# Performance work log

Hardware: AMD Instinct MI355X
Metric: run time of the kernel (lower is better)

The kernel has to match this reference:

```python
import jax, jax.numpy as jnp
import numpy as np


def _lstm_dir(x, W_ih, W_hh, b_ih, b_hh, reverse):
    # x: [T, B, Din] -> hs: [T, B, H]; PyTorch gate order i,f,g,o
    xs = x[::-1] if reverse else x
    gx = xs @ W_ih.T + (b_ih + b_hh)  # [T, B, 4H] precomputed input contribution
    H = W_hh.shape[1]
    B = x.shape[1]

    def step(carry, g):
        h, c = carry
        g = g + h @ W_hh.T
        i, f, gg, o = jnp.split(g, 4, axis=-1)
        c = jax.nn.sigmoid(f) * c + jax.nn.sigmoid(i) * jnp.tanh(gg)
        h = jax.nn.sigmoid(o) * jnp.tanh(c)
        return (h, c), h

    z = jnp.zeros((B, H), x.dtype)
    _, hs = jax.lax.scan(step, (z, z), gx)
    return hs[::-1] if reverse else hs


def _emissions(inputs, emb, layers, W_out, b_out):
    x = jnp.swapaxes(emb[inputs], 0, 1)  # [T, B, E]
    for (Wif, Whf, bif, bhf, Wib, Whb, bib, bhb) in layers:
        hf = _lstm_dir(x, Wif, Whf, bif, bhf, False)
        hb = _lstm_dir(x, Wib, Whb, bib, bhb, True)
        x = jnp.concatenate([hf, hb], axis=-1)  # [T, B, 2H]
    return x @ W_out.T + b_out  # [T, B, K]


def _viterbi(em, start_trans, end_trans, trans):
    # em: [T, B, K] -> (tags [B, T] int32, best_score [B])
    score0 = start_trans + em[0]  # [B, K]

    def fwd_step(score, e):
        s = score[:, :, None] + trans[None, :, :]  # [B, Kprev, Knext]
        bp = jnp.argmax(s, axis=1)
        return jnp.max(s, axis=1) + e, bp

    score, bps = jax.lax.scan(fwd_step, score0, em[1:])  # bps: [T-1, B, K]
    score = score + end_trans
    last_tag = jnp.argmax(score, axis=1)  # [B]
    best_score = jnp.max(score, axis=1)   # [B]

    def back_step(tag, bp):
        prev = jnp.take_along_axis(bp, tag[:, None], axis=1)[:, 0]
        return prev, prev

    _, prevs = jax.lax.scan(back_step, last_tag, bps, reverse=True)  # [T-1, B]
    tags = jnp.concatenate([prevs, last_tag[None]], axis=0)  # [T, B]
    return jnp.swapaxes(tags, 0, 1).astype(jnp.int32), best_score


def setup_inputs() -> dict:
    key = jax.random.key(0)
    ks = jax.random.split(key, 24)
    B, T, V, E, H, K = 64, 512, 30000, 256, 256, 32

    def n(k, shape, s=0.05):
        return jax.random.normal(k, shape, dtype=jnp.float32) * s

    d = {"inputs": jax.random.randint(ks[0], (B, T), 0, V)}
    d["emb"] = n(ks[1], (V, E), 0.1).at[0].set(0.0)  # padding_idx=0
    i = 2
    for l, din in [(0, E), (1, 2 * H)]:
        for dr in ("f", "b"):
            d[f"W_ih_l{l}_{dr}"] = n(ks[i], (4 * H, din)); i += 1
            d[f"W_hh_l{l}_{dr}"] = n(ks[i], (4 * H, H)); i += 1
            d[f"b_ih_l{l}_{dr}"] = n(ks[i], (4 * H,)); i += 1
            d[f"b_hh_l{l}_{dr}"] = n(ks[i], (4 * H,)); i += 1
    d["W_out"] = n(ks[i], (K, 2 * H)); i += 1
    d["b_out"] = n(ks[i], (K,)); i += 1
    d["start_trans"] = n(ks[i], (K,)); i += 1
    d["end_trans"] = n(ks[i], (K,)); i += 1
    d["trans"] = n(ks[i], (K, K)); i += 1
    return d


def reference(inputs, emb,
              W_ih_l0_f, W_hh_l0_f, b_ih_l0_f, b_hh_l0_f,
              W_ih_l0_b, W_hh_l0_b, b_ih_l0_b, b_hh_l0_b,
              W_ih_l1_f, W_hh_l1_f, b_ih_l1_f, b_hh_l1_f,
              W_ih_l1_b, W_hh_l1_b, b_ih_l1_b, b_hh_l1_b,
              W_out, b_out, start_trans, end_trans, trans):
    layers = [
        (W_ih_l0_f, W_hh_l0_f, b_ih_l0_f, b_hh_l0_f,
         W_ih_l0_b, W_hh_l0_b, b_ih_l0_b, b_hh_l0_b),
        (W_ih_l1_f, W_hh_l1_f, b_ih_l1_f, b_hh_l1_f,
         W_ih_l1_b, W_hh_l1_b, b_ih_l1_b, b_hh_l1_b),
    ]
    em = _emissions(inputs, emb, layers, W_out, b_out)
    tags, _ = _viterbi(em, start_trans, end_trans, trans)
    return tags  # [B, T] best tag sequence per batch element
```

## Files before the change

### kernel.cpp

```cpp
#include <hip/hip_runtime.h>
#include <math.h>
#include <stdint.h>

#define TLEN 512
#define BSZ  64
#define EDIM 256
#define HDIM 256
#define GDIM 1024
#define KTAG 32

__device__ __forceinline__ float sigf(float x) { return 1.0f / (1.0f + expf(-x)); }

template<int KDIM, bool GATHER, bool TOXBUF>
__global__ __launch_bounds__(512, 2)
void lstm_fused(
    const float* __restrict__ gx_f, const float* __restrict__ gx_b,
    const float* __restrict__ Wf, const float* __restrict__ Wb,
    float* __restrict__ xout, float* __restrict__ hbuf,
    float* __restrict__ state, uint64_t* __restrict__ hxs,
    unsigned int fbase,
    int t0f, int t0b, int C, int init, int nlstm, int nmt,
    const float* __restrict__ A, const int* __restrict__ idx,
    const float* __restrict__ Bf, const float* __restrict__ Bb,
    const float* __restrict__ b1f, const float* __restrict__ b2f,
    const float* __restrict__ b1b, const float* __restrict__ b2b,
    float* __restrict__ ogx_f, float* __restrict__ ogx_b,
    int gt0f, int gt0b, int gr0f, int gr0b)
{
    __shared__ __align__(16) float h_lds[4][256];
    __shared__ __align__(16) float ps[2][4][256];
    __shared__ __align__(16) float gxs[4][256];
    __shared__ __align__(16) float As[8][132];
    __shared__ __align__(16) float Bs[8][132];

    const int bid = blockIdx.x;
    const int t = threadIdx.x;

    if (bid < nlstm) {
        const int cl  = bid & 31;
        const int rb  = bid >> 5;
        const int dir = cl >> 4;
        const int b0g = (cl & 15) * 4;
        const float* gx = dir ? gx_b : gx_f;
        const float* W  = dir ? Wb : Wf;
        const int t0 = dir ? t0b : t0f;

        const int rr = t & 255;
        const int kh = t >> 8;
        const int urow = ((rr >> 6) * 256) + rb * 64 + (rr & 63);

        float4 w[32];
        {
            const float4* wrow = (const float4*)(W + (size_t)urow * HDIM + kh * 128);
            #pragma unroll
            for (int i = 0; i < 32; ++i) w[i] = wrow[i];
        }
        #pragma unroll
        for (int i = 0; i < 32; ++i)
            asm volatile("" : "+v"(w[i].x), "+v"(w[i].y), "+v"(w[i].z), "+v"(w[i].w));

        float cc = 0.0f;
        for (int i = t; i < 4 * 256; i += 512) {
            int b = i >> 8, u = i & 255;
            h_lds[b][u] = init ? 0.0f
                : state[(((size_t)dir * BSZ + (b0g + b)) * 2) * HDIM + u];
        }
        if (t < 256) {
            int b = t >> 6, ug = rb * 64 + (t & 63);
            if (!init)
                cc = state[(((size_t)dir * BSZ + (b0g + b)) * 2) * HDIM + HDIM + ug];
        }
        __syncthreads();
        __builtin_amdgcn_s_setprio(1);

        for (int s = 0; s < C; ++s) {
            const int tloc = dir ? (C - 1 - s) : s;
            const int idx2 = t * 2;
            const int pb = idx2 >> 8;
            const int rem = idx2 & 255;
            const float* gxp = gx + ((size_t)tloc * BSZ + (b0g + pb)) * GDIM
                             + ((rem >> 6) * 256) + rb * 64 + (rem & 63);
            float2 gv = *(const float2*)gxp;
            float a0 = 0.f, a1 = 0.f, a2 = 0.f, a3 = 0.f;
            #pragma unroll
            for (int i = 0; i < 32; ++i) {
                float4 h0 = *(const float4*)&h_lds[0][kh * 128 + i * 4];
                float4 h1 = *(const float4*)&h_lds[1][kh * 128 + i * 4];
                float4 h2 = *(const float4*)&h_lds[2][kh * 128 + i * 4];
                float4 h3 = *(const float4*)&h_lds[3][kh * 128 + i * 4];
                a0 = fmaf(w[i].x, h0.x, a0); a0 = fmaf(w[i].y, h0.y, a0);
                a0 = fmaf(w[i].z, h0.z, a0); a0 = fmaf(w[i].w, h0.w, a0);
                a1 = fmaf(w[i].x, h1.x, a1); a1 = fmaf(w[i].y, h1.y, a1);
                a1 = fmaf(w[i].z, h1.z, a1); a1 = fmaf(w[i].w, h1.w, a1);
                a2 = fmaf(w[i].x, h2.x, a2); a2 = fmaf(w[i].y, h2.y, a2);
                a2 = fmaf(w[i].z, h2.z, a2); a2 = fmaf(w[i].w, h2.w, a2);
                a3 = fmaf(w[i].x, h3.x, a3); a3 = fmaf(w[i].y, h3.y, a3);
                a3 = fmaf(w[i].z, h3.z, a3); a3 = fmaf(w[i].w, h3.w, a3);
            }
            ps[kh][0][rr] = a0; ps[kh][1][rr] = a1;
            ps[kh][2][rr] = a2; ps[kh][3][rr] = a3;
            gxs[pb][rem] = gv.x; gxs[pb][rem + 1] = gv.y;
            __syncthreads();
            const unsigned want = fbase + (unsigned)(s + 1);
            if (t < 256) {
                const int b = t >> 6, u = t & 63;
                float pi = ps[0][b][u]       + ps[1][b][u]       + gxs[b][u];
                float pf = ps[0][b][64 + u]  + ps[1][b][64 + u]  + gxs[b][64 + u];
                float pg = ps[0][b][128 + u] + ps[1][b][128 + u] + gxs[b][128 + u];
                float po = ps[0][b][192 + u] + ps[1][b][192 + u] + gxs[b][192 + u];
                float iv = sigf(pi), fv = sigf(pf), gv2 = tanhf(pg), ov = sigf(po);
                cc = fv * cc + iv * gv2;
                float hv = ov * tanhf(cc);
                const int ug = rb * 64 + u;
                h_lds[b][ug] = hv;
                uint64_t pv = ((uint64_t)want << 32) | (uint64_t)__float_as_uint(hv);
                __hip_atomic_store(&hxs[(((size_t)(s & 1) * 32 + cl) * 4 + b) * 256 + ug],
                                   pv, __ATOMIC_RELAXED, __HIP_MEMORY_SCOPE_AGENT);
                if (TOXBUF)
                    xout[((size_t)(t0 + tloc) * BSZ + (b0g + b)) * 512 + dir * HDIM + ug] = hv;
                else
                    hbuf[(((size_t)dir * C + tloc) * BSZ + (b0g + b)) * HDIM + ug] = hv;
            }
            __builtin_amdgcn_s_setprio(0);
            #pragma unroll
            for (int q = 0; q < 2; ++q) {
                int i = t * 2 + q;
                int b = i >> 8, u = i & 255;
                if ((u >> 6) != rb) {
                    const uint64_t* src =
                        &hxs[(((size_t)(s & 1) * 32 + cl) * 4 + b) * 256 + u];
                    uint64_t v;
                    do {
                        v = __hip_atomic_load(src, __ATOMIC_RELAXED,
                                              __HIP_MEMORY_SCOPE_AGENT);
                    } while ((unsigned)(v >> 32) != want);
                    h_lds[b][u] = __uint_as_float((unsigned)v);
                }
            }
            __builtin_amdgcn_s_setprio(1);
            __syncthreads();
        }
        __builtin_amdgcn_s_setprio(0);
        if (t < 256) {
            int b = t >> 6, ug = rb * 64 + (t & 63);
            size_t sb = (((size_t)dir * BSZ + (b0g + b)) * 2) * HDIM;
            state[sb + ug] = h_lds[b][ug];
            state[sb + HDIM + ug] = cc;
        }
        return;
    }

    const int g = bid - nlstm;
    const int mx = g % nmt;
    const int ny = g / nmt;
    const int mt = mx * 128;
    const int ngc = ny * 128;
    const bool isF = (ngc < GDIM);
    const int nt = isF ? ngc : (ngc - GDIM);
    const float* Bw = isF ? Bf : Bb;
    const float* bias1 = isF ? b1f : b1b;
    const float* bias2 = isF ? b2f : b2b;
    float* Cc = isF ? ogx_f : ogx_b;
    const int t0 = isF ? gt0f : gt0b;
    const int r0 = isF ? gr0f : gr0b;

    const int tx = t & 15;
    const int ty = t >> 4;
    const int l_row = t >> 2;
    const int l_k = (t & 3) * 2;

    const float* arow;
    if (GATHER) {
        int m = mt + l_row;
        int tt = t0 + (m >> 6);
        int b = m & 63;
        arow = A + (size_t)idx[b * TLEN + tt] * (size_t)KDIM;
    } else {
        arow = A + (size_t)(r0 + mt + l_row) * (size_t)KDIM;
    }
    const float* brow = Bw + (size_t)(nt + l_row) * (size_t)KDIM;

    float acc[4][8];
    #pragma unroll
    for (int i = 0; i < 4; ++i)
        #pragma unroll
        for (int j = 0; j < 8; ++j) acc[i][j] = 0.0f;

    float2 av = *(const float2*)(arow + l_k);
    float2 bv = *(const float2*)(brow + l_k);
    for (int k0 = 0; k0 < KDIM; k0 += 8) {
        __syncthreads();
        As[l_k + 0][l_row] = av.x; As[l_k + 1][l_row] = av.y;
        Bs[l_k + 0][l_row] = bv.x; Bs[l_k + 1][l_row] = bv.y;
        __syncthreads();
        if (k0 + 8 < KDIM) {
            av = *(const float2*)(arow + k0 + 8 + l_k);
            bv = *(const float2*)(brow + k0 + 8 + l_k);
        }
        #pragma unroll
        for (int k = 0; k < 8; ++k) {
            float a[4], bb2[8];
            *(float4*)(a)       = *(const float4*)&As[k][ty * 4];
            *(float4*)(bb2)     = *(const float4*)&Bs[k][tx * 4];
            *(float4*)(bb2 + 4) = *(const float4*)&Bs[k][64 + tx * 4];
            #pragma unroll
            for (int i = 0; i < 4; ++i)
                #pragma unroll
                for (int j = 0; j < 8; ++j)
                    acc[i][j] = fmaf(a[i], bb2[j], acc[i][j]);
        }
    }

    float bs[8];
    #pragma unroll
    for (int j = 0; j < 4; ++j) bs[j] = bias1[nt + tx * 4 + j] + bias2[nt + tx * 4 + j];
    #pragma unroll
    for (int j = 4; j < 8; ++j) bs[j] = bias1[nt + 64 + tx * 4 + j - 4] + bias2[nt + 64 + tx * 4 + j - 4];
    #pragma unroll
    for (int i = 0; i < 4; ++i) {
        size_t row = (size_t)(mt + ty * 4 + i);
        float* cp0 = Cc + row * GDIM + nt + tx * 4;
        float* cp1 = Cc + row * GDIM + nt + 64 + tx * 4;
        *(float4*)cp0 = make_float4(acc[i][0] + bs[0], acc[i][1] + bs[1],
                                    acc[i][2] + bs[2], acc[i][3] + bs[3]);
        *(float4*)cp1 = make_float4(acc[i][4] + bs[4], acc[i][5] + bs[5],
                                    acc[i][6] + bs[6], acc[i][7] + bs[7]);
    }
}

__global__ __launch_bounds__(256)
void emis_part(const float* __restrict__ hbuf, const float* __restrict__ Wo,
               float* __restrict__ em_f, float* __restrict__ em_b,
               int t0f, int t0b, int C)
{
    __shared__ float Ws[128][33];
    const int dir = blockIdx.y;
    const int tid = threadIdx.x;
    const int r = tid >> 5;
    const int kk = tid & 31;
    const int mloc = blockIdx.x * 8 + r;
    const float* hrow = hbuf + ((size_t)dir * C * BSZ + mloc) * HDIM;
    float* emo = dir ? em_b : em_f;
    const int t0 = dir ? t0b : t0f;
    float acc = 0.0f;
    for (int kc = 0; kc < HDIM; kc += 128) {
        __syncthreads();
        for (int i = tid; i < KTAG * 128; i += 256) {
            int wk = i >> 7;
            int k = i & 127;
            Ws[k][wk] = Wo[(size_t)wk * 512 + dir * HDIM + kc + k];
        }
        __syncthreads();
        #pragma unroll 8
        for (int k4 = 0; k4 < 32; ++k4) {
            float4 xv = *(const float4*)(hrow + kc + k4 * 4);
            acc = fmaf(xv.x, Ws[k4 * 4 + 0][kk], acc);
            acc = fmaf(xv.y, Ws[k4 * 4 + 1][kk], acc);
            acc = fmaf(xv.z, Ws[k4 * 4 + 2][kk], acc);
            acc = fmaf(xv.w, Ws[k4 * 4 + 3][kk], acc);
        }
    }
    const int tloc = mloc >> 6;
    const int b = mloc & 63;
    emo[(((size_t)(t0 + tloc)) * BSZ + b) * KTAG + kk] = acc;
}

__global__ __launch_bounds__(64)
void viterbi(const float* __restrict__ em_f, const float* __restrict__ em_b,
             const float* __restrict__ bo,
             const float* __restrict__ st, const float* __restrict__ en,
             const float* __restrict__ tr, int* __restrict__ out)
{
    const int b = blockIdx.x;
    const int lane = threadIdx.x;
    __shared__ float s_tr[KTAG][KTAG + 1];
    __shared__ float s_sc[KTAG];
    __shared__ float s_fin[KTAG];
    __shared__ unsigned char s_bp[TLEN - 1][KTAG];
    for (int i = lane; i < KTAG * KTAG; i += 64)
        s_tr[i >> 5][i & 31] = tr[i];
    float eFn = 0.f, eBn = 0.f;
    if (lane < KTAG) {
        size_t e0 = (size_t)b * KTAG + lane;
        s_sc[lane] = st[lane] + em_f[e0] + em_b[e0] + bo[lane];
        size_t e1 = ((size_t)1 * BSZ + b) * KTAG + lane;
        eFn = em_f[e1]; eBn = em_b[e1];
    }
    __syncthreads();
    for (int t = 1; t < TLEN; ++t) {
        float ecF = eFn, ecB = eBn;
        if (t + 1 < TLEN && lane < KTAG) {
            size_t e2 = ((size_t)(t + 1) * BSZ + b) * KTAG + lane;
            eFn = em_f[e2]; eBn = em_b[e2];
        }
        float best = -3.0e38f;
        int arg = 0;
        if (lane < KTAG) {
            #pragma unroll
            for (int i = 0; i < KTAG; ++i) {
                float c = s_sc[i] + s_tr[i][lane];
                if (c > best) { best = c; arg = i; }
            }
        }
        __syncthreads();
        if (lane < KTAG) {
            s_sc[lane] = best + ecF + ecB + bo[lane];
            s_bp[t - 1][lane] = (unsigned char)arg;
        }
        __syncthreads();
    }
    if (lane < KTAG) s_fin[lane] = s_sc[lane] + en[lane];
    __syncthreads();
    if (lane == 0) {
        int tag = 0;
        float bv = s_fin[0];
        for (int i = 1; i < KTAG; ++i)
            if (s_fin[i] > bv) { bv = s_fin[i]; tag = i; }
        out[(size_t)b * TLEN + (TLEN - 1)] = tag;
        for (int t = TLEN - 2; t >= 0; --t) {
            tag = s_bp[t][tag];
            out[(size_t)b * TLEN + t] = tag;
        }
    }
}

extern "C" void kernel_launch(void* const* d_in, const int* in_sizes, int n_in,
                              void* d_out, int out_size, void* d_ws, size_t ws_size,
                              hipStream_t stream)
{
    (void)in_sizes; (void)n_in; (void)out_size;
    const int*   inputs     = (const int*)d_in[0];
    const float* emb        = (const float*)d_in[1];
    const float* W_ih_l0_f  = (const float*)d_in[2];
    const float* W_hh_l0_f  = (const float*)d_in[3];
    const float* b_ih_l0_f  = (const float*)d_in[4];
    const float* b_hh_l0_f  = (const float*)d_in[5];
    const float* W_ih_l0_b  = (const float*)d_in[6];
    const float* W_hh_l0_b  = (const float*)d_in[7];
    const float* b_ih_l0_b  = (const float*)d_in[8];
    const float* b_hh_l0_b  = (const float*)d_in[9];
    const float* W_ih_l1_f  = (const float*)d_in[10];
    const float* W_hh_l1_f  = (const float*)d_in[11];
    const float* b_ih_l1_f  = (const float*)d_in[12];
    const float* b_hh_l1_f  = (const float*)d_in[13];
    const float* W_ih_l1_b  = (const float*)d_in[14];
    const float* W_hh_l1_b  = (const float*)d_in[15];
    const float* b_ih_l1_b  = (const float*)d_in[16];
    const float* b_hh_l1_b  = (const float*)d_in[17];
    const float* W_out      = (const float*)d_in[18];
    const float* b_out      = (const float*)d_in[19];
    const float* start_tr   = (const float*)d_in[20];
    const float* end_tr     = (const float*)d_in[21];
    const float* trans      = (const float*)d_in[22];

    const size_t XBUF = 67108864ull;
    const size_t PERC = 4ull * 262144 + 131072;
    const size_t TAIL = 2ull * 4194304 + 524288 + 524288;
    int C = 8;
    for (int cand = TLEN; cand >= 8; cand >>= 1) {
        if (XBUF + (size_t)cand * PERC + TAIL <= ws_size) { C = cand; break; }
    }
    char* ws = (char*)d_ws;
    float* xbuf  = (float*)(ws);
    char*  p     = ws + XBUF;
    float* gxA_f = (float*)(p); p += (size_t)C * 262144;
    float* gxA_b = (float*)(p); p += (size_t)C * 262144;
    float* gxB_f = (float*)(p); p += (size_t)C * 262144;
    float* gxB_b = (float*)(p); p += (size_t)C * 262144;
    float* hbuf  = (float*)(p); p += (size_t)C * 131072;
    float* em_f  = (float*)(p); p += 4194304;
    float* em_b  = (float*)(p); p += 4194304;
    float* state = (float*)(p); p += 524288;
    uint64_t* hxs = (uint64_t*)(p);
    int* outi = (int*)d_out;

    const int nc = TLEN / C;
    const int nmt = C / 2;
    const int NG = nmt * 16;
    float* gxf[2] = { gxA_f, gxB_f };
    float* gxb[2] = { gxA_b, gxB_b };

    hipMemsetAsync(hxs, 0, 524288, stream);
    unsigned fbase = 0;

    lstm_fused<EDIM, true, true><<<NG, 512, 0, stream>>>(
        gxA_f, gxA_b, W_hh_l0_f, W_hh_l0_b, xbuf, nullptr, state, hxs, 0,
        0, 0, C, 1, 0, nmt,
        emb, inputs, W_ih_l0_f, W_ih_l0_b,
        b_ih_l0_f, b_hh_l0_f, b_ih_l0_b, b_hh_l0_b,
        gxA_f, gxA_b, 0, TLEN - C, 0, 0);
    for (int c = 0; c < nc; ++c) {
        int cur = c & 1, nxt = cur ^ 1;
        int hasN = (c + 1 < nc);
        int t0f = c * C, t0b = TLEN - (c + 1) * C;
        int g0f = (c + 1) * C, g0b = TLEN - (c + 2) * C;
        lstm_fused<EDIM, true, true><<<128 + (hasN ? NG : 0), 512, 0, stream>>>(
            gxf[cur], gxb[cur], W_hh_l0_f, W_hh_l0_b, xbuf, nullptr, state,
            hxs, fbase, t0f, t0b, C, c == 0 ? 1 : 0, 128, nmt,
            emb, inputs, W_ih_l0_f, W_ih_l0_b,
            b_ih_l0_f, b_hh_l0_f, b_ih_l0_b, b_hh_l0_b,
            gxf[nxt], gxb[nxt], g0f, g0b, 0, 0);
        fbase += (unsigned)C;
    }
    lstm_fused<512, false, false><<<NG, 512, 0, stream>>>(
        gxA_f, gxA_b, W_hh_l1_f, W_hh_l1_b, nullptr, hbuf, state, hxs, 0,
        0, 0, C, 1, 0, nmt,
        xbuf, nullptr, W_ih_l1_f, W_ih_l1_b,
        b_ih_l1_f, b_hh_l1_f, b_ih_l1_b, b_hh_l1_b,
        gxA_f, gxA_b, 0, TLEN - C, 0, (TLEN - C) * BSZ);
    for (int c = 0; c < nc; ++c) {
        int cur = c & 1, nxt = cur ^ 1;
        int hasN = (c + 1 < nc);
        int t0f = c * C, t0b = TLEN - (c + 1) * C;
        int g0f = (c + 1) * C, g0b = TLEN - (c + 2) * C;
        lstm_fused<512, false, false><<<128 + (hasN ? NG : 0), 512, 0, stream>>>(
            gxf[cur], gxb[cur], W_hh_l1_f, W_hh_l1_b, nullptr, hbuf, state,
            hxs, fbase, t0f, t0b, C, c == 0 ? 1 : 0, 128, nmt,
            xbuf, nullptr, W_ih_l1_f, W_ih_l1_b,
            b_ih_l1_f, b_hh_l1_f, b_ih_l1_b, b_hh_l1_b,
            gxf[nxt], gxb[nxt], g0f, g0b, g0f * BSZ, g0b * BSZ);
        fbase += (unsigned)C;
        dim3 ge(C * 8, 2);
        emis_part<<<ge, 256, 0, stream>>>(hbuf, W_out, em_f, em_b, t0f, t0b, C);
    }

    viterbi<<<64, 64, 0, stream>>>(em_f, em_b, b_out, start_tr, end_tr, trans,
                                   outi);
}
```

Before: 4.638 ms.

## Split recurrent LSTM work across 256 blocks with 4-way K split

Doubles the number of persistent recurrent blocks from 128 to 256. Each block now owns 32 hidden units instead of 64, and the K reduction is split four ways with 16 float4 weights per thread instead of 32. This halves per-block register weight storage and per-step FMA work, aiming to shorten the serial per-timestep critical path. In exchange, each block must poll more foreign hidden values from the global exchange buffer, and the reduction adds LDS partial sums.

```diff
diff --git a/kernel.cpp b/kernel.cpp
--- a/kernel.cpp
+++ b/kernel.cpp
@@ -28,8 +28,8 @@
     int gt0f, int gt0b, int gr0f, int gr0b)
 {
     __shared__ __align__(16) float h_lds[4][256];
-    __shared__ __align__(16) float ps[2][4][256];
-    __shared__ __align__(16) float gxs[4][256];
+    __shared__ __align__(16) float ps[4][4][128];
+    __shared__ __align__(16) float gxs[4][128];
     __shared__ __align__(16) float As[8][132];
     __shared__ __align__(16) float Bs[8][132];
 
@@ -45,18 +45,18 @@
         const float* W  = dir ? Wb : Wf;
         const int t0 = dir ? t0b : t0f;
 
-        const int rr = t & 255;
-        const int kh = t >> 8;
-        const int urow = ((rr >> 6) * 256) + rb * 64 + (rr & 63);
-
-        float4 w[32];
+        const int rr = t & 127;
+        const int kq = t >> 7;
+        const int urow = ((rr >> 5) * 256) + rb * 32 + (rr & 31);
+
+        float4 w[16];
         {
-            const float4* wrow = (const float4*)(W + (size_t)urow * HDIM + kh * 128);
+            const float4* wrow = (const float4*)(W + (size_t)urow * HDIM + kq * 64);
             #pragma unroll
-            for (int i = 0; i < 32; ++i) w[i] = wrow[i];
+            for (int i = 0; i < 16; ++i) w[i] = wrow[i];
         }
         #pragma unroll
-        for (int i = 0; i < 32; ++i)
+        for (int i = 0; i < 16; ++i)
             asm volatile("" : "+v"(w[i].x), "+v"(w[i].y), "+v"(w[i].z), "+v"(w[i].w));
 
         float cc = 0.0f;
@@ -65,8 +65,8 @@
             h_lds[b][u] = init ? 0.0f
                 : state[(((size_t)dir * BSZ + (b0g + b)) * 2) * HDIM + u];
         }
-        if (t < 256) {
-            int b = t >> 6, ug = rb * 64 + (t & 63);
+        if (t < 128) {
+            int b = t >> 5, ug = rb * 32 + (t & 31);
             if (!init)
                 cc = state[(((size_t)dir * BSZ + (b0g + b)) * 2) * HDIM + HDIM + ug];
         }
@@ -75,19 +75,15 @@
 
         for (int s = 0; s < C; ++s) {
             const int tloc = dir ? (C - 1 - s) : s;
-            const int idx2 = t * 2;
-            const int pb = idx2 >> 8;
-            const int rem = idx2 & 255;
-            const float* gxp = gx + ((size_t)tloc * BSZ + (b0g + pb)) * GDIM
-                             + ((rem >> 6) * 256) + rb * 64 + (rem & 63);
-            float2 gv = *(const float2*)gxp;
+            const int pb = t >> 7;
+            float gv = gx[((size_t)tloc * BSZ + (b0g + pb)) * GDIM + urow];
             float a0 = 0.f, a1 = 0.f, a2 = 0.f, a3 = 0.f;
             #pragma unroll
-            for (int i = 0; i < 32; ++i) {
-                float4 h0 = *(const float4*)&h_lds[0][kh * 128 + i * 4];
-                float4 h1 = *(const float4*)&h_lds[1][kh * 128 + i * 4];
-                float4 h2 = *(const float4*)&h_lds[2][kh * 128 + i * 4];
-                float4 h3 = *(const float4*)&h_lds[3][kh * 128 + i * 4];
+            for (int i = 0; i < 16; ++i) {
+                float4 h0 = *(const float4*)&h_lds[0][kq * 64 + i * 4];
+                float4 h1 = *(const float4*)&h_lds[1][kq * 64 + i * 4];
+                float4 h2 = *(const float4*)&h_lds[2][kq * 64 + i * 4];
+                float4 h3 = *(const float4*)&h_lds[3][kq * 64 + i * 4];
                 a0 = fmaf(w[i].x, h0.x, a0); a0 = fmaf(w[i].y, h0.y, a0);
                 a0 = fmaf(w[i].z, h0.z, a0); a0 = fmaf(w[i].w, h0.w, a0);
                 a1 = fmaf(w[i].x, h1.x, a1); a1 = fmaf(w[i].y, h1.y, a1);
@@ -97,21 +93,21 @@
                 a3 = fmaf(w[i].x, h3.x, a3); a3 = fmaf(w[i].y, h3.y, a3);
                 a3 = fmaf(w[i].z, h3.z, a3); a3 = fmaf(w[i].w, h3.w, a3);
             }
-            ps[kh][0][rr] = a0; ps[kh][1][rr] = a1;
-            ps[kh][2][rr] = a2; ps[kh][3][rr] = a3;
-            gxs[pb][rem] = gv.x; gxs[pb][rem + 1] = gv.y;
+            ps[kq][0][rr] = a0; ps[kq][1][rr] = a1;
+            ps[kq][2][rr] = a2; ps[kq][3][rr] = a3;
+            gxs[pb][rr] = gv;
             __syncthreads();
             const unsigned want = fbase + (unsigned)(s + 1);
-            if (t < 256) {
-                const int b = t >> 6, u = t & 63;
-                float pi = ps[0][b][u]       + ps[1][b][u]       + gxs[b][u];
-                float pf = ps[0][b][64 + u]  + ps[1][b][64 + u]  + gxs[b][64 + u];
-                float pg = ps[0][b][128 + u] + ps[1][b][128 + u] + gxs[b][128 + u];
-                float po = ps[0][b][192 + u] + ps[1][b][192 + u] + gxs[b][192 + u];
+            if (t < 128) {
+                const int b = t >> 5, ul = t & 31;
+                float pi = ps[0][b][ul]      + ps[1][b][ul]      + ps[2][b][ul]      + ps[3][b][ul]      + gxs[b][ul];
+                float pf = ps[0][b][32 + ul] + ps[1][b][32 + ul] + ps[2][b][32 + ul] + ps[3][b][32 + ul] + gxs[b][32 + ul];
+                float pg = ps[0][b][64 + ul] + ps[1][b][64 + ul] + ps[2][b][64 + ul] + ps[3][b][64 + ul] + gxs[b][64 + ul];
+                float po = ps[0][b][96 + ul] + ps[1][b][96 + ul] + ps[2][b][96 + ul] + ps[3][b][96 + ul] + gxs[b][96 + ul];
                 float iv = sigf(pi), fv = sigf(pf), gv2 = tanhf(pg), ov = sigf(po);
                 cc = fv * cc + iv * gv2;
                 float hv = ov * tanhf(cc);
-                const int ug = rb * 64 + u;
+                const int ug = rb * 32 + ul;
                 h_lds[b][ug] = hv;
                 uint64_t pv = ((uint64_t)want << 32) | (uint64_t)__float_as_uint(hv);
                 __hip_atomic_store(&hxs[(((size_t)(s & 1) * 32 + cl) * 4 + b) * 256 + ug],
@@ -124,9 +120,9 @@
             __builtin_amdgcn_s_setprio(0);
             #pragma unroll
             for (int q = 0; q < 2; ++q) {
-                int i = t * 2 + q;
+                int i = t + q * 512;
                 int b = i >> 8, u = i & 255;
-                if ((u >> 6) != rb) {
+                if ((u >> 5) != rb) {
                     const uint64_t* src =
                         &hxs[(((size_t)(s & 1) * 32 + cl) * 4 + b) * 256 + u];
                     uint64_t v;
@@ -141,8 +137,8 @@
             __syncthreads();
         }
         __builtin_amdgcn_s_setprio(0);
-        if (t < 256) {
-            int b = t >> 6, ug = rb * 64 + (t & 63);
+        if (t < 128) {
+            int b = t >> 5, ug = rb * 32 + (t & 31);
             size_t sb = (((size_t)dir * BSZ + (b0g + b)) * 2) * HDIM;
             state[sb + ug] = h_lds[b][ug];
             state[sb + HDIM + ug] = cc;
@@ -377,6 +373,7 @@
     const int nc = TLEN / C;
     const int nmt = C / 2;
     const int NG = nmt * 16;
+    const int NL = 256;
     float* gxf[2] = { gxA_f, gxB_f };
     float* gxb[2] = { gxA_b, gxB_b };
 
@@ -394,9 +391,9 @@
         int hasN = (c + 1 < nc);
         int t0f = c * C, t0b = TLEN - (c + 1) * C;
         int g0f = (c + 1) * C, g0b = TLEN - (c + 2) * C;
-        lstm_fused<EDIM, true, true><<<128 + (hasN ? NG : 0), 512, 0, stream>>>(
+        lstm_fused<EDIM, true, true><<<NL + (hasN ? NG : 0), 512, 0, stream>>>(
             gxf[cur], gxb[cur], W_hh_l0_f, W_hh_l0_b, xbuf, nullptr, state,
-            hxs, fbase, t0f, t0b, C, c == 0 ? 1 : 0, 128, nmt,
+            hxs, fbase, t0f, t0b, C, c == 0 ? 1 : 0, NL, nmt,
             emb, inputs, W_ih_l0_f, W_ih_l0_b,
             b_ih_l0_f, b_hh_l0_f, b_ih_l0_b, b_hh_l0_b,
             gxf[nxt], gxb[nxt], g0f, g0b, 0, 0);
@@ -413,9 +410,9 @@
         int hasN = (c + 1 < nc);
         int t0f = c * C, t0b = TLEN - (c + 1) * C;
         int g0f = (c + 1) * C, g0b = TLEN - (c + 2) * C;
-        lstm_fused<512, false, false><<<128 + (hasN ? NG : 0), 512, 0, stream>>>(
+        lstm_fused<512, false, false><<<NL + (hasN ? NG : 0), 512, 0, stream>>>(
             gxf[cur], gxb[cur], W_hh_l1_f, W_hh_l1_b, nullptr, hbuf, state,
-            hxs, fbase, t0f, t0b, C, c == 0 ? 1 : 0, 128, nmt,
+            hxs, fbase, t0f, t0b, C, c == 0 ? 1 : 0, NL, nmt,
             xbuf, nullptr, W_ih_l1_f, W_ih_l1_b,
             b_ih_l1_f, b_hh_l1_f, b_ih_l1_b, b_hh_l1_b,
             gxf[nxt], gxb[nxt], g0f, g0b, g0f * BSZ, g0b * BSZ);
```

Measured after the change: 4.801 ms. +3.5%, slower.

## Split LSTM recurrence across 256 blocks with 2 batch rows each and prefetch gx

Applied to the files above, without the earlier changes.

Doubles the number of persistent LSTM blocks from 128 to 256, so each cluster handles 2 batch rows instead of 4. This halves the per-step FMA and LDS work per block and spreads the recurrence over more compute units. The next step's input-gate value is now loaded one step early, overlapping that global load with the exchange wait. In exchange there are twice as many clusters synchronising through the global hxs spin-wait buffer. Fewer blocks remain free for the GEMM tiles launched alongside, and co-residency of all spinning blocks becomes a tighter requirement.

```diff
diff --git a/kernel.cpp b/kernel.cpp
--- a/kernel.cpp
+++ b/kernel.cpp
@@ -27,9 +27,9 @@
     float* __restrict__ ogx_f, float* __restrict__ ogx_b,
     int gt0f, int gt0b, int gr0f, int gr0b)
 {
-    __shared__ __align__(16) float h_lds[4][256];
-    __shared__ __align__(16) float ps[2][4][256];
-    __shared__ __align__(16) float gxs[4][256];
+    __shared__ __align__(16) float h_lds[2][256];
+    __shared__ __align__(16) float ps[2][2][256];
+    __shared__ __align__(16) float gxs[2][256];
     __shared__ __align__(16) float As[8][132];
     __shared__ __align__(16) float Bs[8][132];
 
@@ -37,10 +37,10 @@
     const int t = threadIdx.x;
 
     if (bid < nlstm) {
-        const int cl  = bid & 31;
-        const int rb  = bid >> 5;
-        const int dir = cl >> 4;
-        const int b0g = (cl & 15) * 4;
+        const int cl  = bid & 63;
+        const int rb  = bid >> 6;
+        const int dir = cl >> 5;
+        const int b0g = (cl & 31) * 2;
         const float* gx = dir ? gx_b : gx_f;
         const float* W  = dir ? Wb : Wf;
         const int t0 = dir ? t0b : t0f;
@@ -60,12 +60,12 @@
             asm volatile("" : "+v"(w[i].x), "+v"(w[i].y), "+v"(w[i].z), "+v"(w[i].w));
 
         float cc = 0.0f;
-        for (int i = t; i < 4 * 256; i += 512) {
+        for (int i = t; i < 2 * 256; i += 512) {
             int b = i >> 8, u = i & 255;
             h_lds[b][u] = init ? 0.0f
                 : state[(((size_t)dir * BSZ + (b0g + b)) * 2) * HDIM + u];
         }
-        if (t < 256) {
+        if (t < 128) {
             int b = t >> 6, ug = rb * 64 + (t & 63);
             if (!init)
                 cc = state[(((size_t)dir * BSZ + (b0g + b)) * 2) * HDIM + HDIM + ug];
@@ -73,75 +73,70 @@
         __syncthreads();
         __builtin_amdgcn_s_setprio(1);
 
+        const int pb = t >> 8;
+        {
+            const int tl0 = dir ? (C - 1) : 0;
+        }
+        float gv = gx[((size_t)(dir ? (C - 1) : 0) * BSZ + (b0g + pb)) * GDIM + urow];
+
         for (int s = 0; s < C; ++s) {
             const int tloc = dir ? (C - 1 - s) : s;
-            const int idx2 = t * 2;
-            const int pb = idx2 >> 8;
-            const int rem = idx2 & 255;
-            const float* gxp = gx + ((size_t)tloc * BSZ + (b0g + pb)) * GDIM
-                             + ((rem >> 6) * 256) + rb * 64 + (rem & 63);
-            float2 gv = *(const float2*)gxp;
-            float a0 = 0.f, a1 = 0.f, a2 = 0.f, a3 = 0.f;
+            float a0 = 0.f, a1 = 0.f;
             #pragma unroll
             for (int i = 0; i < 32; ++i) {
                 float4 h0 = *(const float4*)&h_lds[0][kh * 128 + i * 4];
                 float4 h1 = *(const float4*)&h_lds[1][kh * 128 + i * 4];
-                float4 h2 = *(const float4*)&h_lds[2][kh * 128 + i * 4];
-                float4 h3 = *(const float4*)&h_lds[3][kh * 128 + i * 4];
                 a0 = fmaf(w[i].x, h0.x, a0); a0 = fmaf(w[i].y, h0.y, a0);
                 a0 = fmaf(w[i].z, h0.z, a0); a0 = fmaf(w[i].w, h0.w, a0);
                 a1 = fmaf(w[i].x, h1.x, a1); a1 = fmaf(w[i].y, h1.y, a1);
                 a1 = fmaf(w[i].z, h1.z, a1); a1 = fmaf(w[i].w, h1.w, a1);
-                a2 = fmaf(w[i].x, h2.x, a2); a2 = fmaf(w[i].y, h2.y, a2);
-                a2 = fmaf(w[i].z, h2.z, a2); a2 = fmaf(w[i].w, h2.w, a2);
-                a3 = fmaf(w[i].x, h3.x, a3); a3 = fmaf(w[i].y, h3.y, a3);
-                a3 = fmaf(w[i].z, h3.z, a3); a3 = fmaf(w[i].w, h3.w, a3);
             }
             ps[kh][0][rr] = a0; ps[kh][1][rr] = a1;
-            ps[kh][2][rr] = a2; ps[kh][3][rr] = a3;
-            gxs[pb][rem] = gv.x; gxs[pb][rem + 1] = gv.y;
+            gxs[pb][rr] = gv;
             __syncthreads();
             const unsigned want = fbase + (unsigned)(s + 1);
-            if (t < 256) {
-                const int b = t >> 6, u = t & 63;
-                float pi = ps[0][b][u]       + ps[1][b][u]       + gxs[b][u];
-                float pf = ps[0][b][64 + u]  + ps[1][b][64 + u]  + gxs[b][64 + u];
-                float pg = ps[0][b][128 + u] + ps[1][b][128 + u] + gxs[b][128 + u];
-                float po = ps[0][b][192 + u] + ps[1][b][192 + u] + gxs[b][192 + u];
+            if (t < 128) {
+                const int b = t >> 6, ul = t & 63;
+                float pi = ps[0][b][ul]       + ps[1][b][ul]       + gxs[b][ul];
+                float pf = ps[0][b][64 + ul]  + ps[1][b][64 + ul]  + gxs[b][64 + ul];
+                float pg = ps[0][b][128 + ul] + ps[1][b][128 + ul] + gxs[b][128 + ul];
+                float po = ps[0][b][192 + ul] + ps[1][b][192 + ul] + gxs[b][192 + ul];
                 float iv = sigf(pi), fv = sigf(pf), gv2 = tanhf(pg), ov = sigf(po);
                 cc = fv * cc + iv * gv2;
                 float hv = ov * tanhf(cc);
-                const int ug = rb * 64 + u;
+                const int ug = rb * 64 + ul;
                 h_lds[b][ug] = hv;
                 uint64_t pv = ((uint64_t)want << 32) | (uint64_t)__float_as_uint(hv);
-                __hip_atomic_store(&hxs[(((size_t)(s & 1) * 32 + cl) * 4 + b) * 256 + ug],
+                __hip_atomic_store(&hxs[(((size_t)(s & 1) * 64 + cl) * 2 + b) * 256 + ug],
                                    pv, __ATOMIC_RELAXED, __HIP_MEMORY_SCOPE_AGENT);
                 if (TOXBUF)
                     xout[((size_t)(t0 + tloc) * BSZ + (b0g + b)) * 512 + dir * HDIM + ug] = hv;
                 else
                     hbuf[(((size_t)dir * C + tloc) * BSZ + (b0g + b)) * HDIM + ug] = hv;
             }
+            if (s + 1 < C) {
+                const int tl2 = dir ? (C - 2 - s) : (s + 1);
+                gv = gx[((size_t)tl2 * BSZ + (b0g + pb)) * GDIM + urow];
+            }
             __builtin_amdgcn_s_setprio(0);
-            #pragma unroll
-            for (int q = 0; q < 2; ++q) {
-                int i = t * 2 + q;
-                int b = i >> 8, u = i & 255;
-                if ((u >> 6) != rb) {
-                    const uint64_t* src =
-                        &hxs[(((size_t)(s & 1) * 32 + cl) * 4 + b) * 256 + u];
-                    uint64_t v;
-                    do {
-                        v = __hip_atomic_load(src, __ATOMIC_RELAXED,
-                                              __HIP_MEMORY_SCOPE_AGENT);
-                    } while ((unsigned)(v >> 32) != want);
-                    h_lds[b][u] = __uint_as_float((unsigned)v);
-                }
+            if (t < 384) {
+                const int b = t / 192;
+                const int ix = t % 192;
+                const int u = (ix < rb * 64) ? ix : ix + 64;
+                const uint64_t* src =
+                    &hxs[(((size_t)(s & 1) * 64 + cl) * 2 + b) * 256 + u];
+                uint64_t v;
+                do {
+                    v = __hip_atomic_load(src, __ATOMIC_RELAXED,
+                                          __HIP_MEMORY_SCOPE_AGENT);
+                } while ((unsigned)(v >> 32) != want);
+                h_lds[b][u] = __uint_as_float((unsigned)v);
             }
             __builtin_amdgcn_s_setprio(1);
             __syncthreads();
         }
         __builtin_amdgcn_s_setprio(0);
-        if (t < 256) {
+        if (t < 128) {
             int b = t >> 6, ug = rb * 64 + (t & 63);
             size_t sb = (((size_t)dir * BSZ + (b0g + b)) * 2) * HDIM;
             state[sb + ug] = h_lds[b][ug];
@@ -377,6 +372,7 @@
     const int nc = TLEN / C;
     const int nmt = C / 2;
     const int NG = nmt * 16;
+    const int NL = 256;
     float* gxf[2] = { gxA_f, gxB_f };
     float* gxb[2] = { gxA_b, gxB_b };
 
@@ -394,9 +390,9 @@
         int hasN = (c + 1 < nc);
         int t0f = c * C, t0b = TLEN - (c + 1) * C;
         int g0f = (c + 1) * C, g0b = TLEN - (c + 2) * C;
-        lstm_fused<EDIM, true, true><<<128 + (hasN ? NG : 0), 512, 0, stream>>>(
+        lstm_fused<EDIM, true, true><<<NL + (hasN ? NG : 0), 512, 0, stream>>>(
             gxf[cur], gxb[cur], W_hh_l0_f, W_hh_l0_b, xbuf, nullptr, state,
-            hxs, fbase, t0f, t0b, C, c == 0 ? 1 : 0, 128, nmt,
+            hxs, fbase, t0f, t0b, C, c == 0 ? 1 : 0, NL, nmt,
             emb, inputs, W_ih_l0_f, W_ih_l0_b,
             b_ih_l0_f, b_hh_l0_f, b_ih_l0_b, b_hh_l0_b,
             gxf[nxt], gxb[nxt], g0f, g0b, 0, 0);
@@ -413,9 +409,9 @@
         int hasN = (c + 1 < nc);
         int t0f = c * C, t0b = TLEN - (c + 1) * C;
         int g0f = (c + 1) * C, g0b = TLEN - (c + 2) * C;
-        lstm_fused<512, false, false><<<128 + (hasN ? NG : 0), 512, 0, stream>>>(
+        lstm_fused<512, false, false><<<NL + (hasN ? NG : 0), 512, 0, stream>>>(
             gxf[cur], gxb[cur], W_hh_l1_f, W_hh_l1_b, nullptr, hbuf, state,
-            hxs, fbase, t0f, t0b, C, c == 0 ? 1 : 0, 128, nmt,
+            hxs, fbase, t0f, t0b, C, c == 0 ? 1 : 0, NL, nmt,
             xbuf, nullptr, W_ih_l1_f, W_ih_l1_b,
             b_ih_l1_f, b_hh_l1_f, b_ih_l1_b, b_hh_l1_b,
             gxf[nxt], gxb[nxt], g0f, g0b, g0f * BSZ, g0b * BSZ);
```

Result: faster. 4.247 ms (-8.4%).
